# Performance work log

Hardware: AMD Instinct MI355X
Metric: run time of the kernel (lower is better)

## Reference

```python
import jax, jax.numpy as jnp
import numpy as np

ALPHA = 0.2  # LeakyReLU negative slope


def setup_inputs() -> dict:
    key = jax.random.key(0)
    k1, k2, k3 = jax.random.split(key, 3)
    N, F_IN, F_OUT = 8192, 128, 64
    inputs = jax.random.normal(k1, (N, F_IN), dtype=jnp.float32)
    # xavier_uniform with gain=1.414
    limW = 1.414 * np.sqrt(6.0 / (F_IN + F_OUT))
    W = jax.random.uniform(k2, (F_IN, F_OUT), minval=-limW, maxval=limW, dtype=jnp.float32)
    lima = 1.414 * np.sqrt(6.0 / (2 * F_OUT + 1))
    a = jax.random.uniform(k3, (2 * F_OUT, 1), minval=-lima, maxval=lima, dtype=jnp.float32)
    return {"inputs": inputs, "W": W, "a": a}


def reference(inputs, W, a):
    F_OUT = W.shape[1]
    h = inputs @ W  # [N, F_out]
    # The torch code concatenates [h_i, h_j] and dots with a; equivalently
    # split a into a1 (for h_i) and a2 (for h_j): e_ij = LeakyReLU(h_i.a1 + h_j.a2)
    a1 = a[:F_OUT, 0]  # [F_out]
    a2 = a[F_OUT:, 0]  # [F_out]
    f1 = h @ a1  # [N]
    f2 = h @ a2  # [N]
    e = jax.nn.leaky_relu(f1[:, None] + f2[None, :], negative_slope=ALPHA)  # [N, N]
    attention = jax.nn.softmax(e, axis=1)  # dense GAT: softmax over all nodes
    # dropout=0.0 / eval mode -> identity
    feature = attention @ h  # [N, F_out]
    return jax.nn.elu(feature)  # concat=True branch
```

## Files before the change

### kernel.cpp

```cpp
#include <hip/hip_runtime.h>

#define NR    8192
#define ALPHA 0.2f
#define NCH   512
#define CSZ   16

__device__ inline unsigned enc_f32(float f) {
    unsigned u = __float_as_uint(f);
    return (u & 0x80000000u) ? ~u : (u | 0x80000000u);
}
__device__ inline float dec_f32(unsigned u) {
    return __uint_as_float((u & 0x80000000u) ? (u ^ 0x80000000u) : ~u);
}

__global__ __launch_bounds__(256) void kA(
    const float* __restrict__ X, const float* __restrict__ W, const float* __restrict__ aa,
    float* __restrict__ H, float* __restrict__ F1, unsigned* __restrict__ ENC)
{
    __shared__ __align__(16) float xs[16 * 128];
    __shared__ float part[16 * 4 * 64];
    const int tid = threadIdx.x, w = tid >> 6, c = tid & 63;
    const int R0 = blockIdx.x * 16;

    float Wreg[32];
#pragma unroll
    for (int e = 0; e < 32; ++e) Wreg[e] = W[(w * 32 + e) * 64 + c];
    {
        const float4* X4 = (const float4*)(X + R0 * 128);
        float4* xs4 = (float4*)xs;
        xs4[tid] = X4[tid];
        xs4[256 + tid] = X4[256 + tid];
    }
    __syncthreads();

    for (int r = 0; r < 16; ++r) {
        const float4* xr4 = (const float4*)&xs[r * 128 + w * 32];
        float acc = 0.f;
#pragma unroll
        for (int e = 0; e < 8; ++e) {
            float4 xv = xr4[e];
            acc = fmaf(xv.x, Wreg[e * 4 + 0], acc);
            acc = fmaf(xv.y, Wreg[e * 4 + 1], acc);
            acc = fmaf(xv.z, Wreg[e * 4 + 2], acc);
            acc = fmaf(xv.w, Wreg[e * 4 + 3], acc);
        }
        part[(r * 4 + w) * 64 + c] = acc;
    }
    __syncthreads();

    const float a1 = aa[c], a2 = aa[64 + c];
    for (int rr = 0; rr < 4; ++rr) {
        const int r = w * 4 + rr, i = R0 + r;
        float h = part[(r * 4 + 0) * 64 + c] + part[(r * 4 + 1) * 64 + c]
                + part[(r * 4 + 2) * 64 + c] + part[(r * 4 + 3) * 64 + c];
        H[i * 64 + c] = h;
        float v1 = h * a1, v2 = h * a2;
#pragma unroll
        for (int m = 32; m >= 1; m >>= 1) {
            v1 += __shfl_xor(v1, m, 64);
            v2 += __shfl_xor(v2, m, 64);
        }
        if (c == 0) { F1[i] = v1; ENC[i] = enc_f32(v2); }
    }
}

__global__ __launch_bounds__(256) void kB(
    const unsigned* __restrict__ ENC, float* __restrict__ SF2, int* __restrict__ PERM)
{
    __shared__ unsigned cw[4 * 8];
    const int tid = threadIdx.x, bid = blockIdx.x;
    const uint4* E4 = (const uint4*)ENC;

    unsigned long long k64[32];
    {
        const unsigned base = tid * 4;
#pragma unroll
        for (int q = 0; q < 8; ++q) {
            uint4 v = E4[q * 256 + tid];
            const unsigned ib = q * 1024 + base;
            k64[q * 4 + 0] = ((unsigned long long)v.x << 13) | (ib + 0);
            k64[q * 4 + 1] = ((unsigned long long)v.y << 13) | (ib + 1);
            k64[q * 4 + 2] = ((unsigned long long)v.z << 13) | (ib + 2);
            k64[q * 4 + 3] = ((unsigned long long)v.w << 13) | (ib + 3);
        }
    }

    unsigned cnt[8];
#pragma unroll
    for (int jj = 0; jj < 8; ++jj) {
        const int j = bid * 8 + jj;
        const unsigned long long th = ((unsigned long long)ENC[j] << 13) | (unsigned)j;
        unsigned cjj = 0;
#pragma unroll
        for (int q = 0; q < 32; ++q) cjj += (unsigned)(k64[q] < th);
        cnt[jj] = cjj;
    }
#pragma unroll
    for (int jj = 0; jj < 8; ++jj) {
        unsigned v = cnt[jj];
#pragma unroll
        for (int m = 32; m >= 1; m >>= 1) v += (unsigned)__shfl_xor((int)v, m, 64);
        cnt[jj] = v;
    }
    const int w = tid >> 6;
    if ((tid & 63) == 0) {
#pragma unroll
        for (int jj = 0; jj < 8; ++jj) cw[w * 8 + jj] = cnt[jj];
    }
    __syncthreads();
    if (tid < 8) {
        const unsigned r = cw[tid] + cw[8 + tid] + cw[16 + tid] + cw[24 + tid];
        const int j = bid * 8 + tid;
        SF2[r] = dec_f32(ENC[j]);
        PERM[r] = j;
    }
}

__global__ __launch_bounds__(1024) void kC34(
    const float* __restrict__ H, const float* __restrict__ SF2, const int* __restrict__ PERM,
    float4* __restrict__ SPQJ, float* __restrict__ CHPx, float* __restrict__ CHQx,
    float* __restrict__ cs)
{
    __shared__ float preP[1024], preQ[1024];
    __shared__ float scP[NCH], scQ[NCH];
    const int t = threadIdx.x, cb = blockIdx.x;
    const float fm = SF2[NR - 1];
    float accP = 0.f, accQ = 0.f;

    const float4* S4 = (const float4*)(SF2 + t * 8);
    const int4*   P4 = (const int4*)(PERM + t * 8);
    float4 f0 = S4[0], f1v = S4[1];
    int4   j0 = P4[0], j1 = P4[1];
    float sv[8] = { f0.x, f0.y, f0.z, f0.w, f1v.x, f1v.y, f1v.z, f1v.w };
    int   jx[8] = { j0.x, j0.y, j0.z, j0.w, j1.x, j1.y, j1.z, j1.w };

    if (cb < 64) {
#pragma unroll
        for (int e = 0; e < 8; ++e) {
            const float d = sv[e] - fm;
            const float P = __expf(d), Q = __expf(ALPHA * d);
            const float hv = H[jx[e] * 64 + cb];
            accP = fmaf(P, hv, accP);
            accQ = fmaf(Q, hv, accQ);
        }
    } else {
#pragma unroll
        for (int e = 0; e < 8; ++e) {
            const float d = sv[e] - fm;
            const float P = __expf(d), Q = __expf(ALPHA * d);
            SPQJ[t * 8 + e] = make_float4(sv[e], P, Q, __int_as_float(jx[e]));
            accP += P; accQ += Q;
        }
        if (t < NCH) cs[t] = SF2[t * CSZ];
    }

    preP[t] = accP; preQ[t] = accQ;
    __syncthreads();
    float vP = 0.f, vQ = 0.f;
    if (t < NCH) {
        vP = preP[2 * t] + preP[2 * t + 1];
        vQ = preQ[2 * t] + preQ[2 * t + 1];
        scP[t] = vP; scQ[t] = vQ;
    }
    __syncthreads();
    for (int off = 1; off < NCH; off <<= 1) {
        float uP = 0.f, uQ = 0.f;
        if (t < NCH && t >= off) { uP = scP[t - off]; uQ = scQ[t - off]; }
        __syncthreads();
        if (t < NCH) { scP[t] += uP; scQ[t] += uQ; }
        __syncthreads();
    }
    if (t < NCH) {
        const float eP = (t > 0) ? scP[t - 1] : 0.f;
        const float eQ = (t > 0) ? scQ[t - 1] : 0.f;
        CHPx[t * 65 + cb] = eP;
        CHQx[t * 65 + cb] = eQ;
        if (t == NCH - 1) { CHPx[NCH * 65 + cb] = scP[t]; CHQx[NCH * 65 + cb] = scQ[t]; }
    }
}

__global__ __launch_bounds__(256) void kD(
    const float* __restrict__ H, const float* __restrict__ F1, const float* __restrict__ SF2,
    const float4* __restrict__ SPQJ, const float* __restrict__ CHPx,
    const float* __restrict__ CHQx, const float* __restrict__ cs, float* __restrict__ OUT)
{
    __shared__ float sb[NCH];
    const int tid = threadIdx.x, w = tid >> 6, c = tid & 63, bid = blockIdx.x;
    sb[tid] = cs[tid];
    sb[256 + tid] = cs[256 + tid];
    __syncthreads();

    const float fm = SF2[NR - 1];
    const float Ptot = CHPx[NCH * 65 + c], ptot = CHPx[NCH * 65 + 64];
    const int i = bid * 4 + w;

    const float f1 = F1[i];
    const float s = f1 + fm;
    const float mrow = fmaxf(s, ALPHA * s);
    const float A = __expf(s - mrow);
    const float B = __expf(ALPHA * s - mrow);
    const float th = -f1;

    int lo = 0, hi = NCH;
    while (lo < hi) { int mid = (lo + hi) >> 1; if (sb[mid] < th) lo = mid + 1; else hi = mid; }
    const int b = lo > 0 ? lo - 1 : 0;
    const int t0 = b * CSZ;

    float qv = CHQx[b * 65 + c],  pp = CHPx[b * 65 + c];
    float qs = CHQx[b * 65 + 64], ps = CHPx[b * 65 + 64];
#pragma unroll
    for (int tt = 0; tt < CSZ; ++tt) {
        const float4 v = SPQJ[t0 + tt];
        const int jv = __float_as_int(v.w);
        const float hv = H[jv * 64 + c];
        const bool cd = v.x < th;
        const float cP = cd ? v.y : 0.f, cQ = cd ? v.z : 0.f;
        qv = fmaf(cQ, hv, qv); qs += cQ;
        pp = fmaf(cP, hv, pp); ps += cP;
    }
    const float Pvec = Ptot - pp;
    const float pden = ptot - ps;
    const float num = A * Pvec + B * qv;
    const float den = A * pden + B * qs;
    const float feat = num / den;
    OUT[i * 64 + c] = feat > 0.f ? feat : expm1f(feat);
}

extern "C" void kernel_launch(void* const* d_in, const int* in_sizes, int n_in,
                              void* d_out, int out_size, void* d_ws, size_t ws_size,
                              hipStream_t stream) {
    const float* X = (const float*)d_in[0];
    const float* W = (const float*)d_in[1];
    const float* a = (const float*)d_in[2];
    float* OUT = (float*)d_out;

    float*    ws   = (float*)d_ws;
    float*    H    = ws;
    float*    F1   = H + 524288;
    unsigned* ENC  = (unsigned*)(F1 + 8192);
    float*    SF2  = (float*)(ENC + 8192);
    int*      PERM = (int*)(SF2 + 8192);
    float4*   SPQJ = (float4*)(PERM + 8192);
    float*    CHPx = (float*)(SPQJ + 8192);
    float*    CHQx = CHPx + 513 * 65;
    float*    cs   = CHQx + 513 * 65;

    kA  <<<512,  256,  0, stream>>>(X, W, a, H, F1, ENC);
    kB  <<<1024, 256,  0, stream>>>(ENC, SF2, PERM);
    kC34<<<65,   1024, 0, stream>>>(H, SF2, PERM, SPQJ, CHPx, CHQx, cs);
    kD  <<<2048, 256,  0, stream>>>(H, F1, SF2, SPQJ, CHPx, CHQx, cs, OUT);
}
```

Baseline: 42.47 us.

## Fuse chunk prefix-sum kernel into rank kernel via atomic chunk and superchunk sums

Removes the separate 65-block scan kernel. The rank kernel now computes the global max, the P/Q exponentials and the SPQJ/cs tables directly, and scatters P*h and Q*h into per-chunk and per-superchunk sums with atomics. Those accumulators are zeroed inside kA. kD then builds each prefix from up to 16 superchunk sums plus up to 32 chunk sums, and subtracts the excluded elements of the boundary chunk. This drops a low-occupancy launch and its serial scan, at the cost of many float atomics, nondeterministic summation order, and more gather work per row in kD.

```diff
diff --git a/kernel.cpp b/kernel.cpp
--- a/kernel.cpp
+++ b/kernel.cpp
@@ -4,6 +4,8 @@
 #define ALPHA 0.2f
 #define NCH   512
 #define CSZ   16
+#define NSC   16
+#define ZN    (NCH * 65 * 2 + NSC * 65 * 2)
 
 __device__ inline unsigned enc_f32(float f) {
     unsigned u = __float_as_uint(f);
@@ -15,12 +17,16 @@
 
 __global__ __launch_bounds__(256) void kA(
     const float* __restrict__ X, const float* __restrict__ W, const float* __restrict__ aa,
-    float* __restrict__ H, float* __restrict__ F1, unsigned* __restrict__ ENC)
+    float* __restrict__ H, float* __restrict__ F1, unsigned* __restrict__ ENC,
+    float* __restrict__ ZERO)
 {
     __shared__ __align__(16) float xs[16 * 128];
     __shared__ float part[16 * 4 * 64];
     const int tid = threadIdx.x, w = tid >> 6, c = tid & 63;
     const int R0 = blockIdx.x * 16;
+
+    const int g = blockIdx.x * 256 + tid;
+    if (g < ZN) ZERO[g] = 0.f;
 
     float Wreg[32];
 #pragma unroll
@@ -65,18 +71,24 @@
 }
 
 __global__ __launch_bounds__(256) void kB(
-    const unsigned* __restrict__ ENC, float* __restrict__ SF2, int* __restrict__ PERM)
+    const unsigned* __restrict__ ENC, const float* __restrict__ H,
+    float4* __restrict__ SPQJ, float* __restrict__ cs, float* __restrict__ FMf,
+    float* __restrict__ CHPQ, float* __restrict__ SCHPQ)
 {
     __shared__ unsigned cw[4 * 8];
+    __shared__ unsigned rks[8];
+    __shared__ float pqs[8][2];
     const int tid = threadIdx.x, bid = blockIdx.x;
     const uint4* E4 = (const uint4*)ENC;
 
     unsigned long long k64[32];
+    unsigned mx = 0;
     {
         const unsigned base = tid * 4;
 #pragma unroll
         for (int q = 0; q < 8; ++q) {
             uint4 v = E4[q * 256 + tid];
+            mx = max(max(mx, v.x), max(max(v.y, v.z), v.w));
             const unsigned ib = q * 1024 + base;
             k64[q * 4 + 0] = ((unsigned long long)v.x << 13) | (ib + 0);
             k64[q * 4 + 1] = ((unsigned long long)v.y << 13) | (ib + 1);
@@ -84,6 +96,13 @@
             k64[q * 4 + 3] = ((unsigned long long)v.w << 13) | (ib + 3);
         }
     }
+#pragma unroll
+    for (int m = 32; m >= 1; m >>= 1)
+        mx = max(mx, (unsigned)__shfl_xor((int)mx, m, 64));
+    if ((tid & 63) == 0) cw[tid >> 6] = mx;
+    __syncthreads();
+    const float fm = dec_f32(max(max(cw[0], cw[1]), max(cw[2], cw[3])));
+    __syncthreads();
 
     unsigned cnt[8];
 #pragma unroll
@@ -111,78 +130,45 @@
     if (tid < 8) {
         const unsigned r = cw[tid] + cw[8 + tid] + cw[16 + tid] + cw[24 + tid];
         const int j = bid * 8 + tid;
-        SF2[r] = dec_f32(ENC[j]);
-        PERM[r] = j;
-    }
-}
-
-__global__ __launch_bounds__(1024) void kC34(
-    const float* __restrict__ H, const float* __restrict__ SF2, const int* __restrict__ PERM,
-    float4* __restrict__ SPQJ, float* __restrict__ CHPx, float* __restrict__ CHQx,
-    float* __restrict__ cs)
-{
-    __shared__ float preP[1024], preQ[1024];
-    __shared__ float scP[NCH], scQ[NCH];
-    const int t = threadIdx.x, cb = blockIdx.x;
-    const float fm = SF2[NR - 1];
-    float accP = 0.f, accQ = 0.f;
-
-    const float4* S4 = (const float4*)(SF2 + t * 8);
-    const int4*   P4 = (const int4*)(PERM + t * 8);
-    float4 f0 = S4[0], f1v = S4[1];
-    int4   j0 = P4[0], j1 = P4[1];
-    float sv[8] = { f0.x, f0.y, f0.z, f0.w, f1v.x, f1v.y, f1v.z, f1v.w };
-    int   jx[8] = { j0.x, j0.y, j0.z, j0.w, j1.x, j1.y, j1.z, j1.w };
-
-    if (cb < 64) {
-#pragma unroll
-        for (int e = 0; e < 8; ++e) {
-            const float d = sv[e] - fm;
-            const float P = __expf(d), Q = __expf(ALPHA * d);
-            const float hv = H[jx[e] * 64 + cb];
-            accP = fmaf(P, hv, accP);
-            accQ = fmaf(Q, hv, accQ);
-        }
-    } else {
-#pragma unroll
-        for (int e = 0; e < 8; ++e) {
-            const float d = sv[e] - fm;
-            const float P = __expf(d), Q = __expf(ALPHA * d);
-            SPQJ[t * 8 + e] = make_float4(sv[e], P, Q, __int_as_float(jx[e]));
-            accP += P; accQ += Q;
-        }
-        if (t < NCH) cs[t] = SF2[t * CSZ];
-    }
-
-    preP[t] = accP; preQ[t] = accQ;
-    __syncthreads();
-    float vP = 0.f, vQ = 0.f;
-    if (t < NCH) {
-        vP = preP[2 * t] + preP[2 * t + 1];
-        vQ = preQ[2 * t] + preQ[2 * t + 1];
-        scP[t] = vP; scQ[t] = vQ;
-    }
-    __syncthreads();
-    for (int off = 1; off < NCH; off <<= 1) {
-        float uP = 0.f, uQ = 0.f;
-        if (t < NCH && t >= off) { uP = scP[t - off]; uQ = scQ[t - off]; }
-        __syncthreads();
-        if (t < NCH) { scP[t] += uP; scQ[t] += uQ; }
-        __syncthreads();
-    }
-    if (t < NCH) {
-        const float eP = (t > 0) ? scP[t - 1] : 0.f;
-        const float eQ = (t > 0) ? scQ[t - 1] : 0.f;
-        CHPx[t * 65 + cb] = eP;
-        CHQx[t * 65 + cb] = eQ;
-        if (t == NCH - 1) { CHPx[NCH * 65 + cb] = scP[t]; CHQx[NCH * 65 + cb] = scQ[t]; }
+        const float f = dec_f32(ENC[j]);
+        const float d = f - fm;
+        const float P = __expf(d), Q = __expf(ALPHA * d);
+        SPQJ[r] = make_float4(f, P, Q, __int_as_float(j));
+        if ((r & (CSZ - 1)) == 0) cs[r >> 4] = f;
+        rks[tid] = r;
+        pqs[tid][0] = P; pqs[tid][1] = Q;
+    }
+    if (bid == 0 && tid == 0) FMf[0] = fm;
+    __syncthreads();
+
+    const int c = tid & 63;
+#pragma unroll
+    for (int e = 0; e < 2; ++e) {
+        const int jj = w * 2 + e;
+        const int j = bid * 8 + jj;
+        const unsigned r = rks[jj];
+        const float P = pqs[jj][0], Q = pqs[jj][1];
+        const int ch = r >> 4, sc = r >> 9;
+        const float hv = H[j * 64 + c];
+        atomicAdd(&CHPQ[(ch * 65 + c) * 2 + 0], P * hv);
+        atomicAdd(&CHPQ[(ch * 65 + c) * 2 + 1], Q * hv);
+        atomicAdd(&SCHPQ[(sc * 65 + c) * 2 + 0], P * hv);
+        atomicAdd(&SCHPQ[(sc * 65 + c) * 2 + 1], Q * hv);
+        if (c == 0) {
+            atomicAdd(&CHPQ[(ch * 65 + 64) * 2 + 0], P);
+            atomicAdd(&CHPQ[(ch * 65 + 64) * 2 + 1], Q);
+            atomicAdd(&SCHPQ[(sc * 65 + 64) * 2 + 0], P);
+            atomicAdd(&SCHPQ[(sc * 65 + 64) * 2 + 1], Q);
+        }
     }
 }
 
 __global__ __launch_bounds__(256) void kD(
-    const float* __restrict__ H, const float* __restrict__ F1, const float* __restrict__ SF2,
-    const float4* __restrict__ SPQJ, const float* __restrict__ CHPx,
-    const float* __restrict__ CHQx, const float* __restrict__ cs, float* __restrict__ OUT)
+    const float* __restrict__ H, const float* __restrict__ F1,
+    const float4* __restrict__ SPQJ, const float* __restrict__ cs,
+    const float* __restrict__ FMf,
+    const float2* __restrict__ CHPQ2, const float2* __restrict__ SCHPQ2,
+    float* __restrict__ OUT)
 {
     __shared__ float sb[NCH];
     const int tid = threadIdx.x, w = tid >> 6, c = tid & 63, bid = blockIdx.x;
@@ -190,10 +176,8 @@
     sb[256 + tid] = cs[256 + tid];
     __syncthreads();
 
-    const float fm = SF2[NR - 1];
-    const float Ptot = CHPx[NCH * 65 + c], ptot = CHPx[NCH * 65 + 64];
+    const float fm = FMf[0];
     const int i = bid * 4 + w;
-
     const float f1 = F1[i];
     const float s = f1 + fm;
     const float mrow = fmaxf(s, ALPHA * s);
@@ -204,19 +188,32 @@
     int lo = 0, hi = NCH;
     while (lo < hi) { int mid = (lo + hi) >> 1; if (sb[mid] < th) lo = mid + 1; else hi = mid; }
     const int b = lo > 0 ? lo - 1 : 0;
-    const int t0 = b * CSZ;
-
-    float qv = CHQx[b * 65 + c],  pp = CHPx[b * 65 + c];
-    float qs = CHQx[b * 65 + 64], ps = CHPx[b * 65 + 64];
-#pragma unroll
-    for (int tt = 0; tt < CSZ; ++tt) {
-        const float4 v = SPQJ[t0 + tt];
+    const int S = b >> 5;
+
+    float Ptot = 0.f, ptot = 0.f;
+    float pp = 0.f, ps = 0.f, qv = 0.f, qs = 0.f;
+#pragma unroll
+    for (int s2 = 0; s2 < NSC; ++s2) {
+        const float2 v  = SCHPQ2[s2 * 65 + c];
+        const float2 vs = SCHPQ2[s2 * 65 + 64];
+        Ptot += v.x; ptot += vs.x;
+        if (s2 < S) { pp += v.x; ps += vs.x; qv += v.y; qs += vs.y; }
+    }
+    for (int k = S << 5; k <= b; ++k) {
+        const float2 v  = CHPQ2[k * 65 + c];
+        const float2 vs = CHPQ2[k * 65 + 64];
+        pp += v.x; ps += vs.x; qv += v.y; qs += vs.y;
+    }
+    const int t0 = b << 4;
+#pragma unroll
+    for (int e = 0; e < CSZ; ++e) {
+        const float4 v = SPQJ[t0 + e];
         const int jv = __float_as_int(v.w);
         const float hv = H[jv * 64 + c];
-        const bool cd = v.x < th;
-        const float cP = cd ? v.y : 0.f, cQ = cd ? v.z : 0.f;
-        qv = fmaf(cQ, hv, qv); qs += cQ;
-        pp = fmaf(cP, hv, pp); ps += cP;
+        const bool ex = !(v.x < th);
+        const float sP = ex ? v.y : 0.f, sQ = ex ? v.z : 0.f;
+        pp = fmaf(-sP, hv, pp); ps -= sP;
+        qv = fmaf(-sQ, hv, qv); qs -= sQ;
     }
     const float Pvec = Ptot - pp;
     const float pden = ptot - ps;
@@ -234,19 +231,18 @@
     const float* a = (const float*)d_in[2];
     float* OUT = (float*)d_out;
 
-    float*    ws   = (float*)d_ws;
-    float*    H    = ws;
-    float*    F1   = H + 524288;
-    unsigned* ENC  = (unsigned*)(F1 + 8192);
-    float*    SF2  = (float*)(ENC + 8192);
-    int*      PERM = (int*)(SF2 + 8192);
-    float4*   SPQJ = (float4*)(PERM + 8192);
-    float*    CHPx = (float*)(SPQJ + 8192);
-    float*    CHQx = CHPx + 513 * 65;
-    float*    cs   = CHQx + 513 * 65;
-
-    kA  <<<512,  256,  0, stream>>>(X, W, a, H, F1, ENC);
-    kB  <<<1024, 256,  0, stream>>>(ENC, SF2, PERM);
-    kC34<<<65,   1024, 0, stream>>>(H, SF2, PERM, SPQJ, CHPx, CHQx, cs);
-    kD  <<<2048, 256,  0, stream>>>(H, F1, SF2, SPQJ, CHPx, CHQx, cs, OUT);
-}
+    float*    ws    = (float*)d_ws;
+    float*    H     = ws;
+    float*    F1    = H + 524288;
+    unsigned* ENC   = (unsigned*)(F1 + 8192);
+    float*    FMf   = (float*)(ENC + 8192);
+    float*    cs    = FMf + 16;
+    float4*   SPQJ  = (float4*)(cs + 512);
+    float*    CHPQ  = (float*)(SPQJ + 8192);
+    float*    SCHPQ = CHPQ + NCH * 65 * 2;
+
+    kA<<<512,  256, 0, stream>>>(X, W, a, H, F1, ENC, CHPQ);
+    kB<<<1024, 256, 0, stream>>>(ENC, H, SPQJ, cs, FMf, CHPQ, SCHPQ);
+    kD<<<2048, 256, 0, stream>>>(H, F1, SPQJ, cs, FMf,
+                                 (const float2*)CHPQ, (const float2*)SCHPQ, OUT);
+}
```

After: 95.57 us. 2.25x slower.
